# Optimization experiments

Measured on AMD Instinct MI355X. Metric: run time of the kernel, lower is better.

## Reference

```python
import jax, jax.numpy as jnp
import numpy as np

N, A, B, H = 16, 2048, 2048, 64


def setup_inputs() -> dict:
    key = jax.random.key(0)
    k1, k2, k3, k4 = jax.random.split(key, 4)
    query = jax.random.normal(k1, (N, A, H), dtype=jnp.float32)
    key_t = jax.random.normal(k2, (N, B, H), dtype=jnp.float32)
    value = jax.random.normal(k3, (N, B, H), dtype=jnp.float32)
    mask = jax.random.randint(k4, (N, B), 0, 2).astype(bool)  # True = masked out
    return {"query": query, "key": key_t, "value": value, "mask": mask}


def reference(query, key, value, mask):
    # attention_product: scaled dot product -> (n, a, b) logits
    h = query.shape[-1]
    scale = 1.0 / jnp.sqrt(jnp.asarray(h, dtype=query.dtype))
    logit = jnp.einsum("nah,nbh->nab", query, key) * scale
    # mask (n, b) broadcast over query axis; masked positions -> -inf
    logit = jnp.where(mask[:, None, :], -jnp.inf, logit)
    attn = jax.nn.softmax(logit, axis=-1)
    # dropout_rate = 0.0 (eval) -> identity
    context = jnp.einsum("nab,nbh->nah", attn, value)
    return context
```

## Files before the change

kernel.cpp:

```cpp
#include <hip/hip_runtime.h>

#define NB 16
#define AQ 2048
#define BKV 2048
#define HD 64

#define QSCALE 0.18033688f
#define MBIAS -43000.0f
#define DTHR 8.0f

typedef float f32x4 __attribute__((ext_vector_type(4)));
typedef float f32x16 __attribute__((ext_vector_type(16)));
typedef short bf16x8 __attribute__((ext_vector_type(8)));
typedef int int4v __attribute__((ext_vector_type(4)));

__device__ __forceinline__ short f2bf(float f) {
  return __builtin_bit_cast(short, static_cast<__bf16>(f));
}
__device__ __forceinline__ unsigned pk2(float a, float b) {
  unsigned lo = (unsigned short)f2bf(a);
  unsigned hh = (unsigned short)f2bf(b);
  return lo | (hh << 16);
}

__global__ __launch_bounds__(256) void prepack(const float* __restrict__ K,
                                               const float* __restrict__ V,
                                               short* __restrict__ Kb,
                                               short* __restrict__ Vt) {
  if (blockIdx.x < 1024) {
    size_t base = ((size_t)blockIdx.x * 256 + threadIdx.x) * 8;
    f32x4 a = *(const f32x4*)(K + base);
    f32x4 b = *(const f32x4*)(K + base + 4);
    bf16x8 o;
#pragma unroll
    for (int i = 0; i < 4; ++i) {
      o[i] = f2bf(a[i]);
      o[i + 4] = f2bf(b[i]);
    }
    *(bf16x8*)(Kb + base) = o;
  } else {
    unsigned vb = blockIdx.x - 1024;
    int n = vb >> 5;
    int b0 = (vb & 31) * 64;
    int t = threadIdx.x;
    __shared__ short tile[64][68];
    int rb = t >> 4;
    int hc = (t & 15) * 4;
#pragma unroll
    for (int j = 0; j < 4; ++j) {
      int r = rb + 16 * j;
      f32x4 v = *(const f32x4*)(V + ((size_t)n * BKV + b0 + r) * HD + hc);
#pragma unroll
      for (int i = 0; i < 4; ++i) tile[r][hc + i] = f2bf(v[i]);
    }
    __syncthreads();
    int hr = t >> 2;
    int bb = (t & 3) * 16;
    bf16x8 o0, o1;
#pragma unroll
    for (int j = 0; j < 8; ++j) {
      o0[j] = tile[bb + j][hr];
      o1[j] = tile[bb + 8 + j][hr];
    }
    short* dst = Vt + ((size_t)n * HD + hr) * BKV + b0 + bb;
    *(bf16x8*)dst = o0;
    *(bf16x8*)(dst + 8) = o1;
  }
}

template <int PRE>
__global__ __launch_bounds__(256, 4) void attn_fwd(
    const float* __restrict__ Q, const float* __restrict__ K,
    const float* __restrict__ V, const int* __restrict__ M,
    const short* __restrict__ Kb, const short* __restrict__ Vt,
    float* __restrict__ O) {
  unsigned orig = blockIdx.x;
  unsigned wg = (orig & 7u) * 128u + (orig >> 3);
  int n = (int)(wg >> 6);
  int q0 = (int)(wg & 63u) * 32;

  int w = threadIdx.x >> 6;
  int lane = threadIdx.x & 63;
  int hi = lane >> 5;
  int li = lane & 31;

  const float* Qn = Q + (size_t)n * AQ * HD;
  const float* Kn = K + (size_t)n * BKV * HD;
  const float* Vn = V + (size_t)n * BKV * HD;
  const short* Kbn = Kb + (size_t)n * BKV * HD;
  const short* Vtn = Vt + (size_t)n * HD * BKV;
  const int* Mn = M + (size_t)n * BKV;

  __shared__ __align__(16) float pacc[4][32][68];
  __shared__ float Ml[4][2][32];

  bf16x8 qb[4];
#pragma unroll
  for (int ks = 0; ks < 4; ++ks) {
    const float* qp = Qn + (size_t)(q0 + li) * HD + 16 * ks + 8 * hi;
    f32x4 a = *(const f32x4*)qp;
    f32x4 b = *(const f32x4*)(qp + 4);
#pragma unroll
    for (int i = 0; i < 4; ++i) {
      qb[ks][i] = f2bf(a[i] * QSCALE);
      qb[ks][i + 4] = f2bf(b[i] * QSCALE);
    }
  }

  f32x16 acc0 = {};
  f32x16 acc1 = {};
  float m_run = -1e30f;
  float l_run = 0.f;

  const int bstart = w * (BKV / 4);
  for (int b0 = bstart; b0 < bstart + (BKV / 4); b0 += 32) {
    int4v mv[4];
#pragma unroll
    for (int j = 0; j < 4; ++j)
      mv[j] = *(const int4v*)(Mn + b0 + 8 * j + 4 * hi);
    f32x16 st;
#pragma unroll
    for (int j = 0; j < 4; ++j)
#pragma unroll
      for (int r = 0; r < 4; ++r) st[4 * j + r] = mv[j][r] ? MBIAS : 0.f;

    __builtin_amdgcn_s_setprio(1);
#pragma unroll
    for (int ks = 0; ks < 4; ++ks) {
      bf16x8 ka;
      if constexpr (PRE) {
        ka = *(const bf16x8*)(Kbn + (size_t)(b0 + li) * HD + 16 * ks + 8 * hi);
      } else {
        const float* kp = Kn + (size_t)(b0 + li) * HD + 16 * ks + 8 * hi;
        f32x4 k0 = *(const f32x4*)kp;
        f32x4 k1 = *(const f32x4*)(kp + 4);
#pragma unroll
        for (int i = 0; i < 4; ++i) {
          ka[i] = f2bf(k0[i]);
          ka[i + 4] = f2bf(k1[i]);
        }
      }
      st = __builtin_amdgcn_mfma_f32_32x32x16_bf16(ka, qb[ks], st, 0, 0, 0);
    }
    __builtin_amdgcn_s_setprio(0);

    float a0 = fmaxf(fmaxf(st[0], st[1]), st[2]);
    float a1 = fmaxf(fmaxf(st[3], st[4]), st[5]);
    float a2 = fmaxf(fmaxf(st[6], st[7]), st[8]);
    float a3 = fmaxf(fmaxf(st[9], st[10]), st[11]);
    float a4 = fmaxf(fmaxf(st[12], st[13]), st[14]);
    float mt = fmaxf(fmaxf(fmaxf(a0, a1), fmaxf(a2, a3)), fmaxf(a4, st[15]));
    mt = fmaxf(mt, __shfl_xor(mt, 32));

    if (!__all(mt - m_run <= DTHR)) {
      float m_new = fmaxf(m_run, mt);
      float fac = exp2f(m_run - m_new);
      l_run *= fac;
#pragma unroll
      for (int i = 0; i < 16; ++i) {
        acc0[i] *= fac;
        acc1[i] *= fac;
      }
      m_run = m_new;
    }

    float rs = 0.f;
#pragma unroll
    for (int i = 0; i < 16; ++i) {
      float e = exp2f(st[i] - m_run);
      st[i] = e;
      rs += e;
    }
    rs += __shfl_xor(rs, 32);
    l_run += rs;

    unsigned w8[8];
#pragma unroll
    for (int j = 0; j < 8; ++j) w8[j] = pk2(st[2 * j], st[2 * j + 1]);
    auto s02 = __builtin_amdgcn_permlane32_swap((int)w8[0], (int)w8[2], false, false);
    auto s13 = __builtin_amdgcn_permlane32_swap((int)w8[1], (int)w8[3], false, false);
    auto s46 = __builtin_amdgcn_permlane32_swap((int)w8[4], (int)w8[6], false, false);
    auto s57 = __builtin_amdgcn_permlane32_swap((int)w8[5], (int)w8[7], false, false);
    int4v p0 = {static_cast<int>(s02[0]), static_cast<int>(s13[0]),
                static_cast<int>(s02[1]), static_cast<int>(s13[1])};
    int4v p1 = {static_cast<int>(s46[0]), static_cast<int>(s57[0]),
                static_cast<int>(s46[1]), static_cast<int>(s57[1])};
    bf16x8 pb0 = __builtin_bit_cast(bf16x8, p0);
    bf16x8 pb1 = __builtin_bit_cast(bf16x8, p1);

#pragma unroll
    for (int ht = 0; ht < 2; ++ht) {
      bf16x8 va0, va1;
      if constexpr (PRE) {
        const short* vp = Vtn + (size_t)(32 * ht + li) * BKV + b0 + 8 * hi;
        va0 = *(const bf16x8*)vp;
        va1 = *(const bf16x8*)(vp + 16);
      } else {
#pragma unroll
        for (int j = 0; j < 8; ++j) {
          va0[j] = f2bf(Vn[(size_t)(b0 + 8 * hi + j) * HD + 32 * ht + li]);
          va1[j] = f2bf(Vn[(size_t)(b0 + 16 + 8 * hi + j) * HD + 32 * ht + li]);
        }
      }
      __builtin_amdgcn_s_setprio(1);
      if (ht == 0) {
        acc0 = __builtin_amdgcn_mfma_f32_32x32x16_bf16(va0, pb0, acc0, 0, 0, 0);
        acc0 = __builtin_amdgcn_mfma_f32_32x32x16_bf16(va1, pb1, acc0, 0, 0, 0);
      } else {
        acc1 = __builtin_amdgcn_mfma_f32_32x32x16_bf16(va0, pb0, acc1, 0, 0, 0);
        acc1 = __builtin_amdgcn_mfma_f32_32x32x16_bf16(va1, pb1, acc1, 0, 0, 0);
      }
      __builtin_amdgcn_s_setprio(0);
    }
  }

  if (hi == 0) {
    Ml[w][0][li] = m_run;
    Ml[w][1][li] = l_run;
  }
#pragma unroll
  for (int reg = 0; reg < 16; ++reg) {
    int hrow = (reg & 3) + 8 * (reg >> 2) + 4 * hi;
    pacc[w][li][hrow] = acc0[reg];
    pacc[w][li][32 + hrow] = acc1[reg];
  }
  __syncthreads();

  {
    int tid = threadIdx.x;
    int q = tid >> 3;
    int hb = (tid & 7) * 8;
    float m0 = Ml[0][0][q], m1 = Ml[1][0][q];
    float m2 = Ml[2][0][q], m3 = Ml[3][0][q];
    float mmax = fmaxf(fmaxf(m0, m1), fmaxf(m2, m3));
    float f[4] = {exp2f(m0 - mmax), exp2f(m1 - mmax), exp2f(m2 - mmax),
                  exp2f(m3 - mmax)};
    float l = f[0] * Ml[0][1][q] + f[1] * Ml[1][1][q] + f[2] * Ml[2][1][q] +
              f[3] * Ml[3][1][q];
    float inv = 1.0f / l;
    float* op = O + ((size_t)n * AQ + q0 + q) * HD + hb;
#pragma unroll
    for (int t = 0; t < 2; ++t) {
      f32x4 o = {0.f, 0.f, 0.f, 0.f};
#pragma unroll
      for (int ww = 0; ww < 4; ++ww) {
        f32x4 a = *(const f32x4*)&pacc[ww][q][hb + 4 * t];
#pragma unroll
        for (int i = 0; i < 4; ++i) o[i] += f[ww] * a[i];
      }
      f32x4 res;
#pragma unroll
      for (int i = 0; i < 4; ++i) res[i] = o[i] * inv;
      *(f32x4*)(op + 4 * t) = res;
    }
  }
}

extern "C" void kernel_launch(void* const* d_in, const int* in_sizes, int n_in,
                              void* d_out, int out_size, void* d_ws, size_t ws_size,
                              hipStream_t stream) {
  const float* q = (const float*)d_in[0];
  const float* k = (const float*)d_in[1];
  const float* v = (const float*)d_in[2];
  const int* m = (const int*)d_in[3];
  float* o = (float*)d_out;

  const size_t kv_elems = (size_t)NB * BKV * HD;
  const size_t need = kv_elems * 2 * sizeof(short);

  if (ws_size >= need) {
    short* kb = (short*)d_ws;
    short* vt = kb + kv_elems;
    prepack<<<dim3(1536), dim3(256), 0, stream>>>(k, v, kb, vt);
    attn_fwd<1><<<dim3(NB * (AQ / 32)), dim3(256), 0, stream>>>(q, k, v, m, kb, vt, o);
  } else {
    attn_fwd<0><<<dim3(NB * (AQ / 32)), dim3(256), 0, stream>>>(q, k, v, m, nullptr, nullptr, o);
  }
}
```

Before: 147.6 us.

## Double-buffer K loads, pack mask to bits, hoist V loads, relax occupancy

Restructures the attention inner loop so that K fragments for the next tile are prefetched into registers (ping-pong buffers) while the current tile computes. All four V fragments are loaded at the start of each tile. The int mask is packed into 32-bit bitmasks in the prepack kernel, so each tile reads one word instead of sixteen ints. Launch bounds drop from 4 to 3 waves per SIMD to leave room for the extra registers, and the row-sum becomes a tree reduction; this trades occupancy for latency hiding.

```diff
diff --git a/kernel.cpp b/kernel.cpp
--- a/kernel.cpp
+++ b/kernel.cpp
@@ -25,8 +25,10 @@
 
 __global__ __launch_bounds__(256) void prepack(const float* __restrict__ K,
                                                const float* __restrict__ V,
+                                               const int* __restrict__ M,
                                                short* __restrict__ Kb,
-                                               short* __restrict__ Vt) {
+                                               short* __restrict__ Vt,
+                                               unsigned* __restrict__ Mb) {
   if (blockIdx.x < 1024) {
     size_t base = ((size_t)blockIdx.x * 256 + threadIdx.x) * 8;
     f32x4 a = *(const f32x4*)(K + base);
@@ -38,7 +40,7 @@
       o[i + 4] = f2bf(b[i]);
     }
     *(bf16x8*)(Kb + base) = o;
-  } else {
+  } else if (blockIdx.x < 1536) {
     unsigned vb = blockIdx.x - 1024;
     int n = vb >> 5;
     int b0 = (vb & 31) * 64;
@@ -65,15 +67,24 @@
     short* dst = Vt + ((size_t)n * HD + hr) * BKV + b0 + bb;
     *(bf16x8*)dst = o0;
     *(bf16x8*)(dst + 8) = o1;
+  } else {
+    unsigned gw = (blockIdx.x - 1536) * 256 + threadIdx.x;
+    int n = (int)(gw >> 6);
+    int ww = (int)(gw & 63u);
+    const int* src = M + (size_t)n * BKV + ww * 32;
+    unsigned bits = 0;
+#pragma unroll
+    for (int j = 0; j < 32; ++j) bits |= (src[j] ? 1u : 0u) << j;
+    Mb[n * 64 + ww] = bits;
   }
 }
 
 template <int PRE>
-__global__ __launch_bounds__(256, 4) void attn_fwd(
+__global__ __launch_bounds__(256, 3) void attn_fwd(
     const float* __restrict__ Q, const float* __restrict__ K,
     const float* __restrict__ V, const int* __restrict__ M,
     const short* __restrict__ Kb, const short* __restrict__ Vt,
-    float* __restrict__ O) {
+    const unsigned* __restrict__ Mb, float* __restrict__ O) {
   unsigned orig = blockIdx.x;
   unsigned wg = (orig & 7u) * 128u + (orig >> 3);
   int n = (int)(wg >> 6);
@@ -89,6 +100,7 @@
   const float* Vn = V + (size_t)n * BKV * HD;
   const short* Kbn = Kb + (size_t)n * BKV * HD;
   const short* Vtn = Vt + (size_t)n * HD * BKV;
+  const unsigned* Mbn = Mb + (size_t)n * 64;
   const int* Mn = M + (size_t)n * BKV;
 
   __shared__ __align__(16) float pacc[4][32][68];
@@ -113,36 +125,69 @@
   float l_run = 0.f;
 
   const int bstart = w * (BKV / 4);
-  for (int b0 = bstart; b0 < bstart + (BKV / 4); b0 += 32) {
-    int4v mv[4];
-#pragma unroll
-    for (int j = 0; j < 4; ++j)
-      mv[j] = *(const int4v*)(Mn + b0 + 8 * j + 4 * hi);
-    f32x16 st;
-#pragma unroll
-    for (int j = 0; j < 4; ++j)
-#pragma unroll
-      for (int r = 0; r < 4; ++r) st[4 * j + r] = mv[j][r] ? MBIAS : 0.f;
-
-    __builtin_amdgcn_s_setprio(1);
+
+  auto LOADK = [&](int b0, bf16x8(&ka)[4]) {
 #pragma unroll
     for (int ks = 0; ks < 4; ++ks) {
-      bf16x8 ka;
       if constexpr (PRE) {
-        ka = *(const bf16x8*)(Kbn + (size_t)(b0 + li) * HD + 16 * ks + 8 * hi);
+        ka[ks] = *(const bf16x8*)(Kbn + (size_t)(b0 + li) * HD + 16 * ks + 8 * hi);
       } else {
         const float* kp = Kn + (size_t)(b0 + li) * HD + 16 * ks + 8 * hi;
         f32x4 k0 = *(const f32x4*)kp;
         f32x4 k1 = *(const f32x4*)(kp + 4);
 #pragma unroll
         for (int i = 0; i < 4; ++i) {
-          ka[i] = f2bf(k0[i]);
-          ka[i + 4] = f2bf(k1[i]);
+          ka[ks][i] = f2bf(k0[i]);
+          ka[ks][i + 4] = f2bf(k1[i]);
         }
       }
-      st = __builtin_amdgcn_mfma_f32_32x32x16_bf16(ka, qb[ks], st, 0, 0, 0);
-    }
-    __builtin_amdgcn_s_setprio(0);
+    }
+  };
+  auto LOADMB = [&](int b0) -> unsigned {
+    if constexpr (PRE) return Mbn[b0 >> 5];
+    return 0u;
+  };
+
+  auto TILE = [&](int b0, const bf16x8(&ka)[4], unsigned mb) {
+    bf16x8 va0, va1, va2, va3;
+    if constexpr (PRE) {
+      const short* vp0 = Vtn + (size_t)li * BKV + b0 + 8 * hi;
+      const short* vp1 = Vtn + (size_t)(32 + li) * BKV + b0 + 8 * hi;
+      va0 = *(const bf16x8*)vp0;
+      va1 = *(const bf16x8*)(vp0 + 16);
+      va2 = *(const bf16x8*)vp1;
+      va3 = *(const bf16x8*)(vp1 + 16);
+    } else {
+#pragma unroll
+      for (int j = 0; j < 8; ++j) {
+        va0[j] = f2bf(Vn[(size_t)(b0 + 8 * hi + j) * HD + li]);
+        va1[j] = f2bf(Vn[(size_t)(b0 + 16 + 8 * hi + j) * HD + li]);
+        va2[j] = f2bf(Vn[(size_t)(b0 + 8 * hi + j) * HD + 32 + li]);
+        va3[j] = f2bf(Vn[(size_t)(b0 + 16 + 8 * hi + j) * HD + 32 + li]);
+      }
+    }
+
+    f32x16 st;
+    if constexpr (PRE) {
+      unsigned ub = mb >> (4 * hi);
+#pragma unroll
+      for (int r = 0; r < 16; ++r) {
+        int pos = (r & 3) + 8 * (r >> 2);
+        st[r] = ((ub >> pos) & 1u) ? MBIAS : 0.f;
+      }
+    } else {
+      int4v mv[4];
+#pragma unroll
+      for (int j = 0; j < 4; ++j) mv[j] = *(const int4v*)(Mn + b0 + 8 * j + 4 * hi);
+#pragma unroll
+      for (int j = 0; j < 4; ++j)
+#pragma unroll
+        for (int r = 0; r < 4; ++r) st[4 * j + r] = mv[j][r] ? MBIAS : 0.f;
+    }
+
+#pragma unroll
+    for (int ks = 0; ks < 4; ++ks)
+      st = __builtin_amdgcn_mfma_f32_32x32x16_bf16(ka[ks], qb[ks], st, 0, 0, 0);
 
     float a0 = fmaxf(fmaxf(st[0], st[1]), st[2]);
     float a1 = fmaxf(fmaxf(st[3], st[4]), st[5]);
@@ -164,13 +209,13 @@
       m_run = m_new;
     }
 
-    float rs = 0.f;
-#pragma unroll
-    for (int i = 0; i < 16; ++i) {
-      float e = exp2f(st[i] - m_run);
-      st[i] = e;
-      rs += e;
-    }
+#pragma unroll
+    for (int i = 0; i < 16; ++i) st[i] = exp2f(st[i] - m_run);
+    float s0 = (st[0] + st[1]) + (st[2] + st[3]);
+    float s1 = (st[4] + st[5]) + (st[6] + st[7]);
+    float s2 = (st[8] + st[9]) + (st[10] + st[11]);
+    float s3 = (st[12] + st[13]) + (st[14] + st[15]);
+    float rs = (s0 + s1) + (s2 + s3);
     rs += __shfl_xor(rs, 32);
     l_run += rs;
 
@@ -188,30 +233,26 @@
     bf16x8 pb0 = __builtin_bit_cast(bf16x8, p0);
     bf16x8 pb1 = __builtin_bit_cast(bf16x8, p1);
 
-#pragma unroll
-    for (int ht = 0; ht < 2; ++ht) {
-      bf16x8 va0, va1;
-      if constexpr (PRE) {
-        const short* vp = Vtn + (size_t)(32 * ht + li) * BKV + b0 + 8 * hi;
-        va0 = *(const bf16x8*)vp;
-        va1 = *(const bf16x8*)(vp + 16);
-      } else {
-#pragma unroll
-        for (int j = 0; j < 8; ++j) {
-          va0[j] = f2bf(Vn[(size_t)(b0 + 8 * hi + j) * HD + 32 * ht + li]);
-          va1[j] = f2bf(Vn[(size_t)(b0 + 16 + 8 * hi + j) * HD + 32 * ht + li]);
-        }
-      }
-      __builtin_amdgcn_s_setprio(1);
-      if (ht == 0) {
-        acc0 = __builtin_amdgcn_mfma_f32_32x32x16_bf16(va0, pb0, acc0, 0, 0, 0);
-        acc0 = __builtin_amdgcn_mfma_f32_32x32x16_bf16(va1, pb1, acc0, 0, 0, 0);
-      } else {
-        acc1 = __builtin_amdgcn_mfma_f32_32x32x16_bf16(va0, pb0, acc1, 0, 0, 0);
-        acc1 = __builtin_amdgcn_mfma_f32_32x32x16_bf16(va1, pb1, acc1, 0, 0, 0);
-      }
-      __builtin_amdgcn_s_setprio(0);
-    }
+    acc0 = __builtin_amdgcn_mfma_f32_32x32x16_bf16(va0, pb0, acc0, 0, 0, 0);
+    acc0 = __builtin_amdgcn_mfma_f32_32x32x16_bf16(va1, pb1, acc0, 0, 0, 0);
+    acc1 = __builtin_amdgcn_mfma_f32_32x32x16_bf16(va2, pb0, acc1, 0, 0, 0);
+    acc1 = __builtin_amdgcn_mfma_f32_32x32x16_bf16(va3, pb1, acc1, 0, 0, 0);
+  };
+
+  bf16x8 kaA[4], kaB[4];
+  LOADK(bstart, kaA);
+  unsigned mbA = LOADMB(bstart), mbB;
+#pragma unroll 1
+  for (int t = 0; t < 16; t += 2) {
+    const int b0 = bstart + t * 32;
+    LOADK(b0 + 32, kaB);
+    mbB = LOADMB(b0 + 32);
+    TILE(b0, kaA, mbA);
+    if (t < 14) {
+      LOADK(b0 + 64, kaA);
+      mbA = LOADMB(b0 + 64);
+    }
+    TILE(b0 + 32, kaB, mbB);
   }
 
   if (hi == 0) {
@@ -266,14 +307,16 @@
   float* o = (float*)d_out;
 
   const size_t kv_elems = (size_t)NB * BKV * HD;
-  const size_t need = kv_elems * 2 * sizeof(short);
+  const size_t mb_words = (size_t)NB * 64;
+  const size_t need = kv_elems * 2 * sizeof(short) + mb_words * 4;
 
   if (ws_size >= need) {
     short* kb = (short*)d_ws;
     short* vt = kb + kv_elems;
-    prepack<<<dim3(1536), dim3(256), 0, stream>>>(k, v, kb, vt);
-    attn_fwd<1><<<dim3(NB * (AQ / 32)), dim3(256), 0, stream>>>(q, k, v, m, kb, vt, o);
+    unsigned* mb = (unsigned*)(vt + kv_elems);
+    prepack<<<dim3(1540), dim3(256), 0, stream>>>(k, v, m, kb, vt, mb);
+    attn_fwd<1><<<dim3(NB * (AQ / 32)), dim3(256), 0, stream>>>(q, k, v, m, kb, vt, mb, o);
   } else {
-    attn_fwd<0><<<dim3(NB * (AQ / 32)), dim3(256), 0, stream>>>(q, k, v, m, nullptr, nullptr, o);
-  }
-}
+    attn_fwd<0><<<dim3(NB * (AQ / 32)), dim3(256), 0, stream>>>(q, k, v, m, nullptr, nullptr, nullptr, o);
+  }
+}
```

After: 140.9 us. 4.5% less time.
